# Optimization experiments

Measured on AMD Instinct MI355X. Metric: run time of the kernel, lower is better.

## Reference

```python
import jax, jax.numpy as jnp
import numpy as np

# --- LIF neuron (spikingjelly LIFNode, single-step, tau=2.0, hard reset, ATan surrogate) ---
# With zero initial membrane potential, one step gives h = x / tau, spike = heaviside(h - v_th).
ALPHA = 2.0  # ATan surrogate default alpha
TAU = 2.0    # LIFNode default tau
V_TH = 1.0

@jax.custom_vjp
def atan_heaviside(x):
    return (x >= 0.0).astype(x.dtype)

def _ah_fwd(x):
    return (x >= 0.0).astype(x.dtype), x

def _ah_bwd(res, g):
    # d/dx of ATan surrogate: alpha / (2 * (1 + (pi/2 * alpha * x)^2))
    return (g * (ALPHA / (2.0 * (1.0 + (jnp.pi / 2.0 * ALPHA * res) ** 2))),)

atan_heaviside.defvjp(_ah_fwd, _ah_bwd)

def lif(x):
    return atan_heaviside(x / TAU - V_TH)

DIM, NUM_HEADS, TOPK = 256, 8, 4
WT, WH, WW = 2, 4, 4

def setup_inputs() -> dict:
    key = jax.random.key(0)
    k1, k2, k3, k4, k5 = jax.random.split(key, 5)
    T, B, Lt, Lh, Lw, C = 4, 2, 8, 32, 32, DIM
    x = jax.random.normal(k1, (T, B, Lt, Lh, Lw, C), dtype=jnp.float32)
    w_qkv = jax.random.normal(k2, (C, 3 * C), dtype=jnp.float32) * 0.02
    b_qkv = jax.random.normal(k3, (3 * C,), dtype=jnp.float32) * 0.02
    w_proj = jax.random.normal(k4, (C, C), dtype=jnp.float32) * 0.02
    b_proj = jax.random.normal(k5, (C,), dtype=jnp.float32) * 0.02
    return {"x": x, "w_qkv": w_qkv, "b_qkv": b_qkv, "w_proj": w_proj, "b_proj": b_proj}

def reference(x, w_qkv, b_qkv, w_proj, b_proj):
    T, B, Lt, Lh, Lw, C = x.shape
    H = NUM_HEADS
    D = C // H
    scale = D ** -0.5
    lt, lh, lw = Lt // WT, Lh // WH, Lw // WW
    W = WT * WH * WW          # num_wins = 32
    S = lt * lh * lw          # win_size = 256

    # window partition: [T,B,Lt,Lh,Lw,C] -> [T,B,W,S,C]
    xw = x.reshape(T, B, WT, lt, WH, lh, WW, lw, C)
    xw = xw.transpose(0, 1, 2, 4, 6, 3, 5, 7, 8).reshape(T, B, W, S, C)

    # region routing: mean over timesteps and tokens -> [B,W,C]
    region = xw.mean(axis=(0, 3))
    scores = jnp.einsum('bwc,bvc->bwv', region, region) * scale  # [B,W,W]
    idx = jax.lax.top_k(scores, TOPK)[1]                          # [B,W,K] int32

    # qkv projection + spiking activations
    qkv = xw @ w_qkv + b_qkv                                      # [T,B,W,S,3C]
    q, k, v = jnp.split(qkv, 3, axis=-1)
    q, k, v = lif(q), lif(k), lif(v)
    q = q.reshape(T, B, W, S, H, D)
    k = k.reshape(T, B, W, S, H, D)
    v = v.reshape(T, B, W, S, H, D)

    # gather routed KV blocks: k_g[t,b,w,j] = k[t,b,idx[b,w,j]]
    b_ix = jnp.arange(B)[:, None, None]
    k_g = k[:, b_ix, idx].reshape(T, B, W, TOPK * S, H, D)        # [T,B,W,K*S,H,D]
    v_g = v[:, b_ix, idx].reshape(T, B, W, TOPK * S, H, D)

    # linear attention: kv = k^T v, out = q @ kv, normalized by q @ sum(k)
    kv = jnp.einsum('tbwnhd,tbwnhe->tbwhde', k_g, v_g)            # [T,B,W,H,D,D]
    out = jnp.einsum('tbwshd,tbwhde->tbwshe', q, kv)              # [T,B,W,S,H,D]
    den = jnp.einsum('tbwshd,tbwhd->tbwsh', q, k_g.sum(axis=3))[..., None]
    out = out / (den + 1e-6)

    out = out.reshape(T, B, W, S, C) @ w_proj + b_proj

    # window reverse: [T,B,W,S,C] -> [T,B,Lt,Lh,Lw,C]
    out = out.reshape(T, B, WT, WH, WW, lt, lh, lw, C)
    out = out.transpose(0, 1, 2, 5, 3, 6, 4, 7, 8).reshape(T, B, Lt, Lh, Lw, C)
    return out
```

## Files before the change

### kernel.cpp

```cpp
#include <hip/hip_runtime.h>
#include <hip/hip_bf16.h>
#include <stdint.h>

#define NT 4
#define NB 2
#define NW 32
#define NS 256
#define NC 256
#define NH 8
#define ND 32
#define NK 4

typedef unsigned int u32;
typedef unsigned short u16;
typedef __attribute__((ext_vector_type(8))) short bf16x8;
typedef __attribute__((ext_vector_type(4))) float f32x4;

__device__ __forceinline__ int wofs(int w) {
  return (w >> 4) * 4096 + ((w >> 2) & 3) * 256 + (w & 3) * 8;
}
__device__ __forceinline__ int sofs(int s) {
  return ((s >> 6) << 10) + (((s >> 3) & 7) << 5) + (s & 7);
}
__device__ __forceinline__ size_t x_off(int t, int b, int w, int s, int c) {
  return ((size_t)((t * NB + b) * 8192 + wofs(w) + sofs(s))) * NC + c;
}

__device__ __forceinline__ u32 f2bf(float f) {
  union { float f; u32 i; } u; u.f = f;
  return (u.i + 0x7FFFu + ((u.i >> 16) & 1u)) >> 16;
}

__device__ __forceinline__ void gload16(const u16* g, u16* l) {
  __builtin_amdgcn_global_load_lds(
      (const __attribute__((address_space(1))) void*)g,
      (__attribute__((address_space(3))) void*)l, 16, 0, 0);
}

__global__ __launch_bounds__(256) void k_convw(const float* __restrict__ w_qkv,
                                               u16* __restrict__ bt) {
  int i = blockIdx.x * 256 + threadIdx.x;
  int k = i / 768, n = i % 768;
  bt[(size_t)n * 256 + k] = (u16)f2bf(w_qkv[i]);
}

__global__ __launch_bounds__(256) void k_convx(const float* __restrict__ x,
                                               u16* __restrict__ xw,
                                               float* __restrict__ partial) {
  __shared__ float sums[4][4][NC];
  int blk = blockIdx.x;
  int tid = threadIdx.x;
  int g = tid >> 6, c4 = tid & 63;
  size_t base = (size_t)blk * 128;
  float4 s[4];
#pragma unroll
  for (int ww = 0; ww < 4; ++ww) s[ww] = make_float4(0.f, 0.f, 0.f, 0.f);
#pragma unroll
  for (int p = 0; p < 32; ++p) {
    int row = p * 4 + g;
    float4 v = *reinterpret_cast<const float4*>(&x[(base + row) * NC + c4 * 4]);
    uint2 bf;
    bf.x = f2bf(v.x) | (f2bf(v.y) << 16);
    bf.y = f2bf(v.z) | (f2bf(v.w) << 16);
    *reinterpret_cast<uint2*>(&xw[(base + row) * NC + c4 * 4]) = bf;
    int ww = (p & 7) >> 1;
    s[ww].x += v.x; s[ww].y += v.y; s[ww].z += v.z; s[ww].w += v.w;
  }
#pragma unroll
  for (int ww = 0; ww < 4; ++ww)
    *reinterpret_cast<float4*>(&sums[ww][g][c4 * 4]) = s[ww];
  __syncthreads();
  int c = tid;
#pragma unroll
  for (int ww = 0; ww < 4; ++ww)
    partial[((size_t)blk * 4 + ww) * NC + c] =
        sums[ww][0][c] + sums[ww][1][c] + sums[ww][2][c] + sums[ww][3][c];
}

__global__ __launch_bounds__(256) void k_reduce(const float* __restrict__ partial,
                                                float* __restrict__ region) {
  int blk = blockIdx.x;
  int b = blk >> 5, v = blk & 31;
  int c = threadIdx.x;
  int wt = v >> 4, wh = (v >> 2) & 3, ww = v & 3;
  float s = 0.f;
#pragma unroll
  for (int t = 0; t < NT; ++t)
#pragma unroll
    for (int it = 0; it < 4; ++it)
#pragma unroll
      for (int j = 0; j < 2; ++j) {
        int pb = (t * NB + b) * 64 + (wt * 4 + it) * 8 + (wh * 2 + j);
        s += partial[((size_t)pb * 4 + ww) * NC + c];
      }
  region[(size_t)blk * NC + c] = s * (1.0f / 1024.0f);
}

__global__ __launch_bounds__(256) void k_scores(const float* __restrict__ region,
                                                int* __restrict__ idx) {
  __shared__ float rs[NW][NC];
  __shared__ float scval[NW];
  int blk = blockIdx.x;
  int b = blk >> 5, w = blk & 31;
  int tid = threadIdx.x;
  for (int i = tid; i < NW * NC; i += 256)
    rs[i >> 8][i & 255] = region[(size_t)b * NW * NC + i];
  __syncthreads();
  int v = tid >> 3, l8 = tid & 7;
  float sum = 0.f;
  const float* a = rs[w];
  const float* bb = rs[v];
#pragma unroll
  for (int j = 0; j < 32; ++j) sum += a[l8 * 32 + j] * bb[l8 * 32 + j];
  sum += __shfl_xor(sum, 1);
  sum += __shfl_xor(sum, 2);
  sum += __shfl_xor(sum, 4);
  if (l8 == 0) scval[v] = sum * 0.17677669529663687f;
  __syncthreads();
  if (tid == 0) {
    float sc[NW];
#pragma unroll
    for (int j = 0; j < NW; ++j) sc[j] = scval[j];
    for (int kk = 0; kk < NK; ++kk) {
      float best = -__builtin_inff(); int bi = 0;
      for (int j = 0; j < NW; ++j)
        if (sc[j] > best) { best = sc[j]; bi = j; }
      idx[(b * NW + w) * NK + kk] = bi;
      sc[bi] = -__builtin_inff();
    }
  }
}

__global__ __launch_bounds__(256) void k_gemm(const u16* __restrict__ xw,
                                              const u16* __restrict__ bt,
                                              const float* __restrict__ b_qkv,
                                              u32* __restrict__ qb, u32* __restrict__ kb,
                                              u32* __restrict__ vb,
                                              u32* __restrict__ winflag) {
  __shared__ __align__(16) u16 As[2][128 * 32];
  __shared__ __align__(16) u16 Bs[2][128 * 32];
  __shared__ u32 pack[128 * 4];
  __shared__ u32 wfl;

  const int tid = threadIdx.x;
  const int v = (blockIdx.x & 7) * 384 + (blockIdx.x >> 3);
  const int mt = v / 6, nt = v % 6;
  const int m0 = mt * 128, n0 = nt * 128;
  const int wave = tid >> 6, lane = tid & 63;
  const int wr = wave >> 1, wc = wave & 1;

  if (tid == 0) wfl = 0;
  for (int i = tid; i < 128 * 4; i += 256) pack[i] = 0;

  const f32x4 vz = {0.f, 0.f, 0.f, 0.f};
  f32x4 acc[4][4];
#pragma unroll
  for (int m = 0; m < 4; ++m)
#pragma unroll
    for (int n = 0; n < 4; ++n) acc[m][n] = vz;

  auto stage = [&](int buf, int ks) {
    const int k0 = ks * 32;
#pragma unroll
    for (int p = 0; p < 2; ++p) {
      int idx2 = p * 256 + wave * 64 + lane;
      int row = idx2 >> 2, ch = idx2 & 3;
      int lbase = (p * 256 + wave * 64) * 8;
      gload16(&xw[(size_t)(m0 + row) * 256 + k0 + ch * 8], &As[buf][lbase]);
      gload16(&bt[(size_t)(n0 + row) * 256 + k0 + ch * 8], &Bs[buf][lbase]);
    }
  };

  stage(0, 0);
  __syncthreads();
#pragma unroll
  for (int ks = 0; ks < 8; ++ks) {
    const int buf = ks & 1;
    if (ks < 7) stage(buf ^ 1, ks + 1);
    bf16x8 afr[4], bfr[4];
#pragma unroll
    for (int m = 0; m < 4; ++m)
      afr[m] = *reinterpret_cast<const bf16x8*>(
          &As[buf][(wr * 64 + m * 16 + (lane & 15)) * 32 + (lane >> 4) * 8]);
#pragma unroll
    for (int n = 0; n < 4; ++n)
      bfr[n] = *reinterpret_cast<const bf16x8*>(
          &Bs[buf][(wc * 64 + n * 16 + (lane & 15)) * 32 + (lane >> 4) * 8]);
#pragma unroll
    for (int m = 0; m < 4; ++m)
#pragma unroll
      for (int n = 0; n < 4; ++n)
        acc[m][n] = __builtin_amdgcn_mfma_f32_16x16x32_bf16(afr[m], bfr[n], acc[m][n], 0, 0, 0);
    __syncthreads();
  }

  float bias[4];
#pragma unroll
  for (int n = 0; n < 4; ++n) bias[n] = b_qkv[n0 + wc * 64 + n * 16 + (lane & 15)];
#pragma unroll
  for (int m = 0; m < 4; ++m)
#pragma unroll
    for (int n = 0; n < 4; ++n)
#pragma unroll
      for (int r = 0; r < 4; ++r) {
        float vv = acc[m][n][r] + bias[n];
        if (vv >= 2.0f) {
          int row = wr * 64 + m * 16 + (lane >> 4) * 4 + r;
          int colb = wc * 64 + n * 16 + (lane & 15);
          atomicOr(&pack[row * 4 + (colb >> 5)], 1u << (colb & 31));
        }
      }
  __syncthreads();
  u32* dst = (nt < 2) ? qb : (nt < 4) ? kb : vb;
  const int h0 = (nt * 4) & 7;
  u32 anyb = 0;
  for (int i = tid; i < 128 * 4; i += 256) {
    int row = i >> 2, j = i & 3;
    u32 pv = pack[i];
    dst[(size_t)(m0 + row) * NH + h0 + j] = pv;
    if (pv) anyb |= 1u << ((row & 31) >> 3);
  }
  if (anyb) atomicOr(&wfl, anyb);
  __syncthreads();
  if (tid == 0 && wfl) {
    int t = mt >> 7, b = (mt >> 6) & 1, Lt = (mt >> 3) & 7, hh = mt & 7;
    int w0 = (Lt >> 2) * 16 + (hh >> 1) * 4;
    u32 bit = (nt < 2) ? 1u : (nt < 4) ? 2u : 4u;
    for (int ww = 0; ww < 4; ++ww)
      if (wfl & (1u << ww))
        atomicOr(&winflag[(t * NB + b) * NW + w0 + ww], bit);
  }
}

__global__ __launch_bounds__(256) void k_attn(const u32* __restrict__ qb,
                                              const u32* __restrict__ kb,
                                              const u32* __restrict__ vb,
                                              const int* __restrict__ idx,
                                              const u32* __restrict__ winflag,
                                              const float* __restrict__ w_proj,
                                              const float* __restrict__ b_proj,
                                              float* __restrict__ out) {
  __shared__ u32 qs[64 * NH];
  __shared__ unsigned short kvc[NH * ND * ND];
  __shared__ u32 ksum[NH * ND];
  __shared__ float attnrow[NC];

  int blk = blockIdx.x;
  int wid = blk >> 2, sc = blk & 3;
  int t = wid >> 6, b = (wid >> 5) & 1, w = wid & 31;
  int s0 = sc * 64;
  int tid = threadIdx.x;

  u32 fs = winflag[(t * NB + b) * NW + w];
  int wj[NK];
  u32 fk = 0, fv = 0;
#pragma unroll
  for (int j = 0; j < NK; ++j) {
    wj[j] = idx[(b * NW + w) * NK + j];
    u32 f = winflag[(t * NB + b) * NW + wj[j]];
    fk |= f & 2u; fv |= f & 4u;
  }
  bool skip = !(fs & 1u) || !fk || !fv;

  if (skip) {
    float bp = b_proj[tid];
    for (int s = s0; s < s0 + 64; ++s) out[x_off(t, b, w, s, tid)] = bp;
    return;
  }

  int tb = (t * NB + b) * 8192;
  size_t gb[NK];
#pragma unroll
  for (int j = 0; j < NK; ++j) gb[j] = (size_t)(tb + wofs(wj[j])) * NH;
  size_t qbase = (size_t)(tb + wofs(w)) * NH;
  for (int i = tid; i < 64 * NH; i += 256)
    qs[i] = qb[qbase + (size_t)sofs(s0 + (i >> 3)) * NH + (i & 7)];
  {
    int h = tid >> 5, d = tid & 31;
    u32 cnt = 0;
    for (int n = 0; n < NK * NS; ++n)
      cnt += (kb[gb[n >> 8] + (size_t)sofs(n & 255) * NH + h] >> d) & 1u;
    ksum[tid] = cnt;
  }
  for (int p = tid; p < NH * ND * ND; p += 256) {
    int h = p >> 10, d = (p >> 5) & 31, e = p & 31;
    u32 cnt = 0;
    for (int n = 0; n < NK * NS; ++n) {
      size_t a = gb[n >> 8] + (size_t)sofs(n & 255) * NH + h;
      cnt += ((kb[a] >> d) & (vb[a] >> e)) & 1u;
    }
    kvc[p] = (unsigned short)cnt;
  }
  __syncthreads();
  int h = tid >> 5, e = tid & 31;
  float bpv = b_proj[tid];
  for (int sl = 0; sl < 64; ++sl) {
    u32 qw = qs[sl * NH + h];
    float num = 0.f, den = 0.f;
    for (int d = 0; d < ND; ++d) {
      if ((qw >> d) & 1u) {
        den += (float)ksum[h * ND + d];
        num += (float)kvc[h * ND * ND + d * ND + e];
      }
    }
    attnrow[tid] = num / (den + 1e-6f);
    __syncthreads();
    float acc = bpv;
    for (int c = 0; c < NC; ++c) acc += attnrow[c] * w_proj[c * NC + tid];
    out[x_off(t, b, w, s0 + sl, tid)] = acc;
    __syncthreads();
  }
}

extern "C" void kernel_launch(void* const* d_in, const int* in_sizes, int n_in,
                              void* d_out, int out_size, void* d_ws, size_t ws_size,
                              hipStream_t stream) {
  const float* x      = (const float*)d_in[0];
  const float* w_qkv  = (const float*)d_in[1];
  const float* b_qkv  = (const float*)d_in[2];
  const float* w_proj = (const float*)d_in[3];
  const float* b_proj = (const float*)d_in[4];
  float* out = (float*)d_out;

  char* ws = (char*)d_ws;
  float* partial = (float*)ws;
  int* idx       = (int*)(ws + 0x200000);
  u16* bt        = (u16*)(ws + 0x201000);
  u32* winflag   = (u32*)(ws + 0x270000);
  float* region  = (float*)(ws + 0x280000);
  u32* qb        = (u32*)(ws + 0x300000);
  u32* kb        = qb + (size_t)NT * NB * NW * NS * NH;
  u32* vb        = kb + (size_t)NT * NB * NW * NS * NH;
  u16* xw        = (u16*)(ws + 0x900000);

  hipMemsetAsync(winflag, 0, NT * NB * NW * sizeof(u32), stream);
  k_convw<<<768, 256, 0, stream>>>(w_qkv, bt);
  k_convx<<<512, 256, 0, stream>>>(x, xw, partial);
  k_reduce<<<NB * NW, 256, 0, stream>>>(partial, region);
  k_scores<<<NB * NW, 256, 0, stream>>>(region, idx);
  k_gemm<<<3072, 256, 0, stream>>>(xw, bt, b_qkv, qb, kb, vb, winflag);
  k_attn<<<NT * NB * NW * 4, 256, 0, stream>>>(qb, kb, vb, idx, winflag, w_proj, b_proj, out);
}
```

Before: 94.26 us.

## Fuse prep kernels, swizzle GEMM LDS tiles, and ballot-pack spike bits

Merges the weight conversion, x conversion and region reduction into one kernel. The region means are now accumulated with float atomics into a memset buffer, which removes two launches and the partial-sum round trip. The GEMM LDS tiles get an XOR swizzle on the 16-byte chunks to cut bank conflicts on the fragment reads. The spike bit-packing now uses wave ballots instead of shared-memory atomicOr. The atomic region sum makes the float summation order nondeterministic, and the weight-conversion part runs on only 4 blocks.

```diff
diff --git a/kernel.cpp b/kernel.cpp
--- a/kernel.cpp
+++ b/kernel.cpp
@@ -12,6 +12,7 @@
 #define NK 4
 
 typedef unsigned int u32;
+typedef unsigned long long u64;
 typedef unsigned short u16;
 typedef __attribute__((ext_vector_type(8))) short bf16x8;
 typedef __attribute__((ext_vector_type(4))) float f32x4;
@@ -37,19 +38,20 @@
       (__attribute__((address_space(3))) void*)l, 16, 0, 0);
 }
 
-__global__ __launch_bounds__(256) void k_convw(const float* __restrict__ w_qkv,
-                                               u16* __restrict__ bt) {
-  int i = blockIdx.x * 256 + threadIdx.x;
-  int k = i / 768, n = i % 768;
-  bt[(size_t)n * 256 + k] = (u16)f2bf(w_qkv[i]);
-}
-
-__global__ __launch_bounds__(256) void k_convx(const float* __restrict__ x,
-                                               u16* __restrict__ xw,
-                                               float* __restrict__ partial) {
+__global__ __launch_bounds__(256) void k_prep(const float* __restrict__ x,
+                                              const float* __restrict__ w_qkv,
+                                              u16* __restrict__ xw,
+                                              u16* __restrict__ bt,
+                                              float* __restrict__ region) {
+  int blk = blockIdx.x, tid = threadIdx.x;
+  if (blk >= 512) {
+    for (int i = (blk - 512) * 256 + tid; i < 256 * 768; i += 1024) {
+      int k = i / 768, n = i % 768;
+      bt[(size_t)n * 256 + k] = (u16)f2bf(w_qkv[i]);
+    }
+    return;
+  }
   __shared__ float sums[4][4][NC];
-  int blk = blockIdx.x;
-  int tid = threadIdx.x;
   int g = tid >> 6, c4 = tid & 63;
   size_t base = (size_t)blk * 128;
   float4 s[4];
@@ -70,30 +72,16 @@
   for (int ww = 0; ww < 4; ++ww)
     *reinterpret_cast<float4*>(&sums[ww][g][c4 * 4]) = s[ww];
   __syncthreads();
+  int b = (blk >> 6) & 1;
+  int wt = ((blk >> 3) & 7) >> 2, wh = (blk & 7) >> 1;
+  int v0 = wt * 16 + wh * 4;
   int c = tid;
 #pragma unroll
-  for (int ww = 0; ww < 4; ++ww)
-    partial[((size_t)blk * 4 + ww) * NC + c] =
-        sums[ww][0][c] + sums[ww][1][c] + sums[ww][2][c] + sums[ww][3][c];
-}
-
-__global__ __launch_bounds__(256) void k_reduce(const float* __restrict__ partial,
-                                                float* __restrict__ region) {
-  int blk = blockIdx.x;
-  int b = blk >> 5, v = blk & 31;
-  int c = threadIdx.x;
-  int wt = v >> 4, wh = (v >> 2) & 3, ww = v & 3;
-  float s = 0.f;
-#pragma unroll
-  for (int t = 0; t < NT; ++t)
-#pragma unroll
-    for (int it = 0; it < 4; ++it)
-#pragma unroll
-      for (int j = 0; j < 2; ++j) {
-        int pb = (t * NB + b) * 64 + (wt * 4 + it) * 8 + (wh * 2 + j);
-        s += partial[((size_t)pb * 4 + ww) * NC + c];
-      }
-  region[(size_t)blk * NC + c] = s * (1.0f / 1024.0f);
+  for (int ww = 0; ww < 4; ++ww) {
+    float tot = (sums[ww][0][c] + sums[ww][1][c] + sums[ww][2][c] + sums[ww][3][c]) *
+                (1.0f / 1024.0f);
+    atomicAdd(&region[((size_t)b * NW + v0 + ww) * NC + c], tot);
+  }
 }
 
 __global__ __launch_bounds__(256) void k_scores(const float* __restrict__ region,
@@ -139,7 +127,6 @@
                                               u32* __restrict__ winflag) {
   __shared__ __align__(16) u16 As[2][128 * 32];
   __shared__ __align__(16) u16 Bs[2][128 * 32];
-  __shared__ u32 pack[128 * 4];
   __shared__ u32 wfl;
 
   const int tid = threadIdx.x;
@@ -150,7 +137,6 @@
   const int wr = wave >> 1, wc = wave & 1;
 
   if (tid == 0) wfl = 0;
-  for (int i = tid; i < 128 * 4; i += 256) pack[i] = 0;
 
   const f32x4 vz = {0.f, 0.f, 0.f, 0.f};
   f32x4 acc[4][4];
@@ -164,10 +150,11 @@
 #pragma unroll
     for (int p = 0; p < 2; ++p) {
       int idx2 = p * 256 + wave * 64 + lane;
-      int row = idx2 >> 2, ch = idx2 & 3;
+      int row = idx2 >> 2, sl = idx2 & 3;
+      int ssl = sl ^ ((row >> 1) & 3);
       int lbase = (p * 256 + wave * 64) * 8;
-      gload16(&xw[(size_t)(m0 + row) * 256 + k0 + ch * 8], &As[buf][lbase]);
-      gload16(&bt[(size_t)(n0 + row) * 256 + k0 + ch * 8], &Bs[buf][lbase]);
+      gload16(&xw[(size_t)(m0 + row) * 256 + k0 + ssl * 8], &As[buf][lbase]);
+      gload16(&bt[(size_t)(n0 + row) * 256 + k0 + ssl * 8], &Bs[buf][lbase]);
     }
   };
 
@@ -179,13 +166,17 @@
     if (ks < 7) stage(buf ^ 1, ks + 1);
     bf16x8 afr[4], bfr[4];
 #pragma unroll
-    for (int m = 0; m < 4; ++m)
-      afr[m] = *reinterpret_cast<const bf16x8*>(
-          &As[buf][(wr * 64 + m * 16 + (lane & 15)) * 32 + (lane >> 4) * 8]);
-#pragma unroll
-    for (int n = 0; n < 4; ++n)
-      bfr[n] = *reinterpret_cast<const bf16x8*>(
-          &Bs[buf][(wc * 64 + n * 16 + (lane & 15)) * 32 + (lane >> 4) * 8]);
+    for (int m = 0; m < 4; ++m) {
+      int r = wr * 64 + m * 16 + (lane & 15);
+      int phys = (lane >> 4) ^ ((r >> 1) & 3);
+      afr[m] = *reinterpret_cast<const bf16x8*>(&As[buf][r * 32 + phys * 8]);
+    }
+#pragma unroll
+    for (int n = 0; n < 4; ++n) {
+      int r = wc * 64 + n * 16 + (lane & 15);
+      int phys = (lane >> 4) ^ ((r >> 1) & 3);
+      bfr[n] = *reinterpret_cast<const bf16x8*>(&Bs[buf][r * 32 + phys * 8]);
+    }
 #pragma unroll
     for (int m = 0; m < 4; ++m)
 #pragma unroll
@@ -197,30 +188,31 @@
   float bias[4];
 #pragma unroll
   for (int n = 0; n < 4; ++n) bias[n] = b_qkv[n0 + wc * 64 + n * 16 + (lane & 15)];
-#pragma unroll
-  for (int m = 0; m < 4; ++m)
-#pragma unroll
-    for (int n = 0; n < 4; ++n)
-#pragma unroll
-      for (int r = 0; r < 4; ++r) {
-        float vv = acc[m][n][r] + bias[n];
-        if (vv >= 2.0f) {
-          int row = wr * 64 + m * 16 + (lane >> 4) * 4 + r;
-          int colb = wc * 64 + n * 16 + (lane & 15);
-          atomicOr(&pack[row * 4 + (colb >> 5)], 1u << (colb & 31));
-        }
-      }
-  __syncthreads();
   u32* dst = (nt < 2) ? qb : (nt < 4) ? kb : vb;
   const int h0 = (nt * 4) & 7;
-  u32 anyb = 0;
-  for (int i = tid; i < 128 * 4; i += 256) {
-    int row = i >> 2, j = i & 3;
-    u32 pv = pack[i];
-    dst[(size_t)(m0 + row) * NH + h0 + j] = pv;
-    if (pv) anyb |= 1u << ((row & 31) >> 3);
-  }
-  if (anyb) atomicOr(&wfl, anyb);
+  const int g = lane >> 4;
+  u32 wfl_loc = 0;
+#pragma unroll
+  for (int m = 0; m < 4; ++m)
+#pragma unroll
+    for (int r = 0; r < 4; ++r) {
+      u32 words[2];
+#pragma unroll
+      for (int np = 0; np < 2; ++np) {
+        u64 b0 = __ballot(acc[m][2 * np][r] + bias[2 * np] >= 2.0f);
+        u64 b1 = __ballot(acc[m][2 * np + 1][r] + bias[2 * np + 1] >= 2.0f);
+        words[np] = (u32)((b0 >> (g * 16)) & 0xFFFFu) |
+                    ((u32)((b1 >> (g * 16)) & 0xFFFFu) << 16);
+      }
+      if ((lane & 15) < 2) {
+        int np = lane & 1;
+        int row = wr * 64 + m * 16 + g * 4 + r;
+        u32 wv = words[np];
+        dst[(size_t)(m0 + row) * NH + h0 + wc * 2 + np] = wv;
+        if (wv) wfl_loc |= 1u << ((row & 31) >> 3);
+      }
+    }
+  if (wfl_loc) atomicOr(&wfl, wfl_loc);
   __syncthreads();
   if (tid == 0 && wfl) {
     int t = mt >> 7, b = (mt >> 6) & 1, Lt = (mt >> 3) & 7, hh = mt & 7;
@@ -323,20 +315,17 @@
   float* out = (float*)d_out;
 
   char* ws = (char*)d_ws;
-  float* partial = (float*)ws;
   int* idx       = (int*)(ws + 0x200000);
   u16* bt        = (u16*)(ws + 0x201000);
   u32* winflag   = (u32*)(ws + 0x270000);
-  float* region  = (float*)(ws + 0x280000);
+  float* region  = (float*)(ws + 0x271000);
   u32* qb        = (u32*)(ws + 0x300000);
   u32* kb        = qb + (size_t)NT * NB * NW * NS * NH;
   u32* vb        = kb + (size_t)NT * NB * NW * NS * NH;
   u16* xw        = (u16*)(ws + 0x900000);
 
-  hipMemsetAsync(winflag, 0, NT * NB * NW * sizeof(u32), stream);
-  k_convw<<<768, 256, 0, stream>>>(w_qkv, bt);
-  k_convx<<<512, 256, 0, stream>>>(x, xw, partial);
-  k_reduce<<<NB * NW, 256, 0, stream>>>(partial, region);
+  hipMemsetAsync(ws + 0x270000, 0, 0x11000, stream);
+  k_prep<<<516, 256, 0, stream>>>(x, w_qkv, xw, bt, region);
   k_scores<<<NB * NW, 256, 0, stream>>>(region, idx);
   k_gemm<<<3072, 256, 0, stream>>>(xw, bt, b_qkv, qb, kb, vb, winflag);
   k_attn<<<NT * NB * NW * 4, 256, 0, stream>>>(qb, kb, vb, idx, winflag, w_proj, b_proj, out);
```

Result: slower. 130.3 us (+38.2%).
